# Performance work log

Hardware: AMD Instinct MI355X
Metric: run time of the kernel (lower is better)

## Reference

```python
import jax, jax.numpy as jnp
import numpy as np

B, C, H, W = 8, 2048, 14, 14
NUM_CLASSES, WORD_DIM, INTER_DIM = 80, 300, 1024


def setup_inputs() -> dict:
    key = jax.random.key(0)
    ks = jax.random.split(key, 8)
    s = 0.02
    return {
        "image_features": jax.random.normal(ks[0], (B, C, H, W), jnp.float32),
        "word_features": jax.random.normal(ks[1], (NUM_CLASSES, WORD_DIM), jnp.float32),
        "W1": jax.random.normal(ks[2], (INTER_DIM, C), jnp.float32) * s,
        "W2": jax.random.normal(ks[3], (INTER_DIM, WORD_DIM), jnp.float32) * s,
        "W3": jax.random.normal(ks[4], (INTER_DIM, INTER_DIM), jnp.float32) * s,
        "b3": jax.random.normal(ks[5], (INTER_DIM,), jnp.float32) * s,
        "Wa": jax.random.normal(ks[6], (1, INTER_DIM), jnp.float32) * s,
        "ba": jax.random.normal(ks[7], (1,), jnp.float32) * s,
        "num_classes": NUM_CLASSES,
    }


def reference(image_features, word_features, W1, W2, W3, b3, Wa, ba, num_classes):
    b, c, h, w = image_features.shape
    # [s, b, c] with s = h*w (spatial locations)
    img = image_features.reshape(b, c, h * w).transpose(2, 0, 1)
    f_wh = img @ W1.T                      # [s, b, D]
    f_wd = word_features @ W2.T            # [n, D]
    # additive-attention score MLP; broadcast to [s, b, n, D]
    lb = jnp.tanh(f_wh[:, :, None, :] * f_wd[None, None, :, :]) @ W3.T + b3
    coef = (lb @ Wa.T + ba)[..., 0]        # [s, b, n]
    coef = jax.nn.softmax(coef, axis=0)    # softmax over spatial locations
    # weighted sum over spatial dim -> [b, n, c]
    return jnp.einsum('sbc,sbn->bnc', img, coef)
```

## Files before the change

### kernel.cpp

```cpp
#include <hip/hip_runtime.h>
#include <math.h>

#define SB 196
#define SP 224
#define NB 8
#define NC 2048
#define ND 1024
#define NN 80
#define NW 300
#define CH 4
#define DCH (ND / CH)

typedef __bf16 v8bf __attribute__((ext_vector_type(8)));
typedef __bf16 v4bf __attribute__((ext_vector_type(4)));
typedef __bf16 v2bf __attribute__((ext_vector_type(2)));
typedef float  f32x4 __attribute__((ext_vector_type(4)));

__global__ __launch_bounds__(256) void k0_v(const float* __restrict__ W3,
                                            const float* __restrict__ Wa,
                                            float* __restrict__ v) {
    int d  = blockIdx.x * 256 + threadIdx.x;
    int e0 = blockIdx.y * 64;
    float p = 0.f;
    #pragma unroll 8
    for (int e = e0; e < e0 + 64; ++e) {
        p += Wa[e] * W3[(size_t)e * ND + d];
    }
    atomicAdd(&v[d], p);
}

__global__ __launch_bounds__(256) void k0_fwd(const float* __restrict__ word,
                                              const float* __restrict__ W2,
                                              const float* __restrict__ v,
                                              float2* __restrict__ wpack) {
    __shared__ __align__(16) float lword[NW];
    int n = blockIdx.x;
    int d = blockIdx.y * 256 + threadIdx.x;
    for (int i = threadIdx.x; i < NW; i += 256) lword[i] = word[(size_t)n * NW + i];
    __syncthreads();
    const float4* wr = (const float4*)(W2 + (size_t)d * NW);
    const float4* l4 = (const float4*)lword;
    float acc = 0.f;
    #pragma unroll 5
    for (int i = 0; i < NW / 4; ++i) {
        float4 a = wr[i], b = l4[i];
        acc += a.x * b.x + a.y * b.y + a.z * b.z + a.w * b.w;
    }
    float2 o;
    o.x = 2.8853900817779268f * acc;
    o.y = -2.f * v[d];
    wpack[(size_t)n * ND + d] = o;
}

__global__ __launch_bounds__(256) void kcast_w1(const float* __restrict__ W1,
                                                __bf16* __restrict__ O) {
    size_t i = ((size_t)blockIdx.x * 256 + threadIdx.x) * 4;
    float4 f = *(const float4*)(W1 + i);
    v4bf o;
    o[0] = (__bf16)f.x; o[1] = (__bf16)f.y; o[2] = (__bf16)f.z; o[3] = (__bf16)f.w;
    *(v4bf*)(O + i) = o;
}

__global__ __launch_bounds__(256) void kcast_x(const float* __restrict__ X,
                                               __bf16* __restrict__ Xt) {
    __shared__ float tile[64][65];
    const int b  = blockIdx.z;
    const int c0 = blockIdx.x * 64;
    const int s0 = blockIdx.y * 64;
    const int t  = threadIdx.x;
    const float* Xb = X + (size_t)b * NC * SB;
    {
        int ss = t & 63, cbase = t >> 6;
        #pragma unroll
        for (int r = 0; r < 16; ++r) {
            int cc = cbase + 4 * r;
            float val = (s0 + ss < SB) ? Xb[(size_t)(c0 + cc) * SB + s0 + ss] : 0.f;
            tile[cc][ss] = val;
        }
    }
    __syncthreads();
    {
        int cc = t & 63, sbase = t >> 6;
        #pragma unroll
        for (int r = 0; r < 16; ++r) {
            int ss = sbase + 4 * r;
            if (s0 + ss < SB)
                Xt[((size_t)b * SB + s0 + ss) * NC + c0 + cc] = (__bf16)tile[cc][ss];
        }
    }
}

#define PITCH 40
__global__ __launch_bounds__(256) void k1_mfma(const __bf16* __restrict__ Xt,
                                               const __bf16* __restrict__ W1b,
                                               float* __restrict__ F) {
    __shared__ __align__(16) __bf16 lA[64 * PITCH];
    __shared__ __align__(16) __bf16 lB[64 * PITCH];
    const int t    = threadIdx.x;
    const int d0   = blockIdx.x * 64;
    const int s0   = blockIdx.y * 64;
    const int b    = blockIdx.z;
    const int lane = t & 63;
    const int wave = t >> 6;
    const int doff = (wave & 1) * 32;
    const int soff = (wave >> 1) * 32;
    const int quad = lane >> 4;
    const int l16  = lane & 15;

    f32x4 acc[2][2] = {};

    const int rr = t >> 2;
    const int cc = (t & 3) * 8;
    const bool sv = (s0 + rr) < SB;
    const __bf16* Ag = W1b + (size_t)(d0 + rr) * NC + cc;
    const __bf16* Bg = Xt + ((size_t)b * SB + (sv ? (s0 + rr) : 0)) * NC + cc;
    __bf16* lAw = lA + rr * PITCH + cc;
    __bf16* lBw = lB + rr * PITCH + cc;

    const __bf16* rA0 = lA + (doff + l16) * PITCH + quad * 8;
    const __bf16* rA1 = rA0 + 16 * PITCH;
    const __bf16* rB0 = lB + (soff + l16) * PITCH + quad * 8;
    const __bf16* rB1 = rB0 + 16 * PITCH;

    for (int k0 = 0; k0 < NC; k0 += 32) {
        uint4 a = *(const uint4*)(Ag + k0);
        uint4 bv = sv ? *(const uint4*)(Bg + k0) : make_uint4(0u, 0u, 0u, 0u);
        __syncthreads();
        *(uint4*)lAw = a;
        *(uint4*)lBw = bv;
        __syncthreads();
        v8bf a0 = *(const v8bf*)rA0;
        v8bf a1 = *(const v8bf*)rA1;
        v8bf b0 = *(const v8bf*)rB0;
        v8bf b1 = *(const v8bf*)rB1;
        acc[0][0] = __builtin_amdgcn_mfma_f32_16x16x32_bf16(a0, b0, acc[0][0], 0, 0, 0);
        acc[0][1] = __builtin_amdgcn_mfma_f32_16x16x32_bf16(a0, b1, acc[0][1], 0, 0, 0);
        acc[1][0] = __builtin_amdgcn_mfma_f32_16x16x32_bf16(a1, b0, acc[1][0], 0, 0, 0);
        acc[1][1] = __builtin_amdgcn_mfma_f32_16x16x32_bf16(a1, b1, acc[1][1], 0, 0, 0);
    }
    float* Fb = F + (size_t)b * ND * SB;
    #pragma unroll
    for (int i = 0; i < 2; ++i) {
        #pragma unroll
        for (int j = 0; j < 2; ++j) {
            int s = s0 + soff + j * 16 + l16;
            if (s < SB) {
                #pragma unroll
                for (int r = 0; r < 4; ++r) {
                    int d = d0 + doff + i * 16 + quad * 4 + r;
                    Fb[(size_t)d * SB + s] = acc[i][j][r];
                }
            }
        }
    }
}

__global__ __launch_bounds__(256) void k2a(const float* __restrict__ F,
                                           const float2* __restrict__ wpack,
                                           float* __restrict__ part) {
    const int n  = blockIdx.x;
    const int b  = blockIdx.y;
    const int ch = blockIdx.z;
    const int t  = threadIdx.x;
    const int sc = (t < SB) ? t : (SB - 1);
    const float*  Fp = F + ((size_t)b * ND + ch * DCH) * SB + sc;
    const float2* wp = wpack + (size_t)n * ND + ch * DCH;
    float acc = 0.f;
    #pragma unroll 8
    for (int d = 0; d < DCH; ++d) {
        float2 w = wp[d];
        float x = Fp[(size_t)d * SB] * w.x;
        float e = __builtin_amdgcn_exp2f(x);
        float r = __builtin_amdgcn_rcpf(1.f + e);
        acc = fmaf(w.y, r, acc);
    }
    part[(((size_t)ch * NB + b) * NN + n) * 256 + t] = acc;
}

__global__ __launch_bounds__(256) void k2b(const float* __restrict__ part,
                                           __bf16* __restrict__ coefh,
                                           __bf16* __restrict__ coefl) {
    __shared__ float red[256];
    const int n = blockIdx.x;
    const int b = blockIdx.y;
    const int t = threadIdx.x;
    float acc = 0.f;
    #pragma unroll
    for (int ch = 0; ch < CH; ++ch)
        acc += part[(((size_t)ch * NB + b) * NN + n) * 256 + t];

    red[t] = (t < SB) ? acc : -1e30f;
    __syncthreads();
    #pragma unroll
    for (int off = 128; off > 0; off >>= 1) {
        if (t < off) red[t] = fmaxf(red[t], red[t + off]);
        __syncthreads();
    }
    float m = red[0];
    __syncthreads();
    float p = (t < SB) ? __expf(acc - m) : 0.f;
    red[t] = p;
    __syncthreads();
    #pragma unroll
    for (int off = 128; off > 0; off >>= 1) {
        if (t < off) red[t] += red[t + off];
        __syncthreads();
    }
    float inv = 1.f / red[0];
    if (t < SP) {
        float val = (t < SB) ? p * inv : 0.f;
        __bf16 h = (__bf16)val;
        __bf16 l = (__bf16)(val - (float)h);
        size_t base = ((size_t)b * NN + n) * SP + t;
        coefh[base] = h;
        coefl[base] = l;
    }
}

__global__ __launch_bounds__(256) void kcast_xs(const float* __restrict__ X,
                                                __bf16* __restrict__ Xhi,
                                                __bf16* __restrict__ Xlo) {
    unsigned int i = blockIdx.x * 256 + threadIdx.x;
    unsigned int row = i / 112;
    int s2 = (int)(i % 112) * 2;
    float x0 = 0.f, x1 = 0.f;
    if (s2 < SB) {
        float2 x = *(const float2*)(X + (size_t)row * SB + s2);
        x0 = x.x; x1 = x.y;
    }
    __bf16 h0 = (__bf16)x0, h1 = (__bf16)x1;
    __bf16 l0 = (__bf16)(x0 - (float)h0), l1 = (__bf16)(x1 - (float)h1);
    v2bf hv; hv[0] = h0; hv[1] = h1;
    v2bf lv; lv[0] = l0; lv[1] = l1;
    *(v2bf*)(Xhi + (size_t)row * SP + s2) = hv;
    *(v2bf*)(Xlo + (size_t)row * SP + s2) = lv;
}

__global__ __launch_bounds__(256) void k3_mfma(const __bf16* __restrict__ Xhi,
                                               const __bf16* __restrict__ Xlo,
                                               const __bf16* __restrict__ coefh,
                                               const __bf16* __restrict__ coefl,
                                               float* __restrict__ out) {
    const int t     = threadIdx.x;
    const int wave  = t >> 6;
    const int lane  = t & 63;
    const int quad  = lane >> 4;
    const int l16   = lane & 15;
    const int b     = blockIdx.y;
    const int cbase = blockIdx.x * 64 + wave * 16;

    const __bf16* Bh = Xhi + ((size_t)b * NC + cbase + l16) * SP + quad * 8;
    const __bf16* Bl = Xlo + ((size_t)b * NC + cbase + l16) * SP + quad * 8;
    const __bf16* Ah = coefh + ((size_t)b * NN + l16) * SP + quad * 8;
    const __bf16* Al = coefl + ((size_t)b * NN + l16) * SP + quad * 8;

    f32x4 acc[5] = {};

    #pragma unroll
    for (int k0 = 0; k0 < SP; k0 += 32) {
        v8bf bh = *(const v8bf*)(Bh + k0);
        v8bf bl = *(const v8bf*)(Bl + k0);
        #pragma unroll
        for (int mt = 0; mt < 5; ++mt) {
            v8bf ah = *(const v8bf*)(Ah + (size_t)mt * 16 * SP + k0);
            v8bf al = *(const v8bf*)(Al + (size_t)mt * 16 * SP + k0);
            acc[mt] = __builtin_amdgcn_mfma_f32_16x16x32_bf16(ah, bh, acc[mt], 0, 0, 0);
            acc[mt] = __builtin_amdgcn_mfma_f32_16x16x32_bf16(al, bh, acc[mt], 0, 0, 0);
            acc[mt] = __builtin_amdgcn_mfma_f32_16x16x32_bf16(ah, bl, acc[mt], 0, 0, 0);
        }
    }
    #pragma unroll
    for (int mt = 0; mt < 5; ++mt) {
        #pragma unroll
        for (int r = 0; r < 4; ++r) {
            int n = mt * 16 + quad * 4 + r;
            out[((size_t)b * NN + n) * NC + cbase + l16] = acc[mt][r];
        }
    }
}

extern "C" void kernel_launch(void* const* d_in, const int* in_sizes, int n_in,
                              void* d_out, int out_size, void* d_ws, size_t ws_size,
                              hipStream_t stream) {
    const float* X    = (const float*)d_in[0];
    const float* word = (const float*)d_in[1];
    const float* W1   = (const float*)d_in[2];
    const float* W2   = (const float*)d_in[3];
    const float* W3   = (const float*)d_in[4];
    const float* Wa   = (const float*)d_in[6];
    float* out = (float*)d_out;

    char* ws = (char*)d_ws;
    float*  v     = (float*)ws;
    float2* wpack = (float2*)(v + ND);
    float*  part  = (float*)(wpack + (size_t)NN * ND);
    __bf16* coefh = (__bf16*)(part + (size_t)CH * NB * NN * 256);
    __bf16* coefl = coefh + (size_t)NB * NN * SP;
    size_t big_off = ((size_t)((char*)(coefl + (size_t)NB * NN * SP) - ws) + 255) & ~(size_t)255;
    char* big = ws + big_off;
    __bf16* W1b = (__bf16*)big;
    __bf16* Xt  = W1b + (size_t)ND * NC;
    float*  F   = (float*)(Xt + (size_t)NB * SB * NC);
    __bf16* Xhi = (__bf16*)big;
    __bf16* Xlo = Xhi + (size_t)NB * NC * SP;

    hipMemsetAsync(v, 0, ND * sizeof(float), stream);
    k0_v    <<<dim3(4, 16),                 256, 0, stream>>>(W3, Wa, v);
    k0_fwd  <<<dim3(NN, 4),                 256, 0, stream>>>(word, W2, v, wpack);
    kcast_w1<<<dim3((ND * NC) / (256 * 4)), 256, 0, stream>>>(W1, W1b);
    kcast_x <<<dim3(32, 4, NB),             256, 0, stream>>>(X, Xt);
    k1_mfma <<<dim3(16, 4, NB),             256, 0, stream>>>(Xt, W1b, F);
    k2a     <<<dim3(NN, NB, CH),            256, 0, stream>>>(F, wpack, part);
    k2b     <<<dim3(NN, NB),                256, 0, stream>>>(part, coefh, coefl);
    kcast_xs<<<dim3((NB * NC * (SP / 2)) / 256), 256, 0, stream>>>(X, Xhi, Xlo);
    k3_mfma <<<dim3(NC / 64, NB),           256, 0, stream>>>(Xhi, Xlo, coefh, coefl, out);
}
```

Before: 198.9 us.

## Fuse hi/lo X split into transpose kernel and pack k2a threads densely

The bf16 hi/lo split of X is now produced inside the transposing cast kernel from the shared tile, which removes the separate kcast_xs pass and its extra read of X. k2a maps threads over flattened (batch, spatial) indices so no lanes sit idle on padding, and it loads weight pairs as float4 with a two-way unrolled inner loop. Xhi/Xlo no longer alias the W1b/Xt/F region, which increases workspace use.

```diff
diff --git a/kernel.cpp b/kernel.cpp
--- a/kernel.cpp
+++ b/kernel.cpp
@@ -62,7 +62,9 @@
 }
 
 __global__ __launch_bounds__(256) void kcast_x(const float* __restrict__ X,
-                                               __bf16* __restrict__ Xt) {
+                                               __bf16* __restrict__ Xt,
+                                               __bf16* __restrict__ Xhi,
+                                               __bf16* __restrict__ Xlo) {
     __shared__ float tile[64][65];
     const int b  = blockIdx.z;
     const int c0 = blockIdx.x * 64;
@@ -86,6 +88,22 @@
             int ss = sbase + 4 * r;
             if (s0 + ss < SB)
                 Xt[((size_t)b * SB + s0 + ss) * NC + c0 + cc] = (__bf16)tile[cc][ss];
+        }
+    }
+    {
+        int ss = t & 63, cbase = t >> 6;
+        int sg = s0 + ss;
+        #pragma unroll
+        for (int r = 0; r < 16; ++r) {
+            int cc = cbase + 4 * r;
+            if (sg < SP) {
+                float val = (sg < SB) ? tile[cc][ss] : 0.f;
+                __bf16 h = (__bf16)val;
+                __bf16 l = (__bf16)(val - (float)h);
+                size_t base = ((size_t)b * NC + c0 + cc) * SP + sg;
+                Xhi[base] = h;
+                Xlo[base] = l;
+            }
         }
     }
 }
@@ -158,23 +176,30 @@
 __global__ __launch_bounds__(256) void k2a(const float* __restrict__ F,
                                            const float2* __restrict__ wpack,
                                            float* __restrict__ part) {
-    const int n  = blockIdx.x;
-    const int b  = blockIdx.y;
-    const int ch = blockIdx.z;
-    const int t  = threadIdx.x;
-    const int sc = (t < SB) ? t : (SB - 1);
-    const float*  Fp = F + ((size_t)b * ND + ch * DCH) * SB + sc;
-    const float2* wp = wpack + (size_t)n * ND + ch * DCH;
+    const int n   = blockIdx.x;
+    const int ch  = blockIdx.z;
+    const int idx = blockIdx.y * 256 + threadIdx.x;
+    const bool valid = idx < (NB * SB);
+    const int iv = valid ? idx : 0;
+    const int b  = iv / SB;
+    const int s  = iv - b * SB;
+    const float*  Fp  = F + ((size_t)b * ND + ch * DCH) * SB + s;
+    const float4* wp4 = (const float4*)(wpack + (size_t)n * ND + ch * DCH);
     float acc = 0.f;
-    #pragma unroll 8
-    for (int d = 0; d < DCH; ++d) {
-        float2 w = wp[d];
-        float x = Fp[(size_t)d * SB] * w.x;
-        float e = __builtin_amdgcn_exp2f(x);
-        float r = __builtin_amdgcn_rcpf(1.f + e);
-        acc = fmaf(w.y, r, acc);
-    }
-    part[(((size_t)ch * NB + b) * NN + n) * 256 + t] = acc;
+    #pragma unroll 4
+    for (int d2 = 0; d2 < DCH / 2; ++d2) {
+        float4 w = wp4[d2];
+        float x0 = Fp[(size_t)(2 * d2)     * SB] * w.x;
+        float x1 = Fp[(size_t)(2 * d2 + 1) * SB] * w.z;
+        float e0 = __builtin_amdgcn_exp2f(x0);
+        float e1 = __builtin_amdgcn_exp2f(x1);
+        float r0 = __builtin_amdgcn_rcpf(1.f + e0);
+        float r1 = __builtin_amdgcn_rcpf(1.f + e1);
+        acc = fmaf(w.y, r0, acc);
+        acc = fmaf(w.w, r1, acc);
+    }
+    if (valid)
+        part[(((size_t)ch * NB + b) * NN + n) * 256 + s] = acc;
 }
 
 __global__ __launch_bounds__(256) void k2b(const float* __restrict__ part,
@@ -215,25 +240,6 @@
         coefh[base] = h;
         coefl[base] = l;
     }
-}
-
-__global__ __launch_bounds__(256) void kcast_xs(const float* __restrict__ X,
-                                                __bf16* __restrict__ Xhi,
-                                                __bf16* __restrict__ Xlo) {
-    unsigned int i = blockIdx.x * 256 + threadIdx.x;
-    unsigned int row = i / 112;
-    int s2 = (int)(i % 112) * 2;
-    float x0 = 0.f, x1 = 0.f;
-    if (s2 < SB) {
-        float2 x = *(const float2*)(X + (size_t)row * SB + s2);
-        x0 = x.x; x1 = x.y;
-    }
-    __bf16 h0 = (__bf16)x0, h1 = (__bf16)x1;
-    __bf16 l0 = (__bf16)(x0 - (float)h0), l1 = (__bf16)(x1 - (float)h1);
-    v2bf hv; hv[0] = h0; hv[1] = h1;
-    v2bf lv; lv[0] = l0; lv[1] = l1;
-    *(v2bf*)(Xhi + (size_t)row * SP + s2) = hv;
-    *(v2bf*)(Xlo + (size_t)row * SP + s2) = lv;
 }
 
 __global__ __launch_bounds__(256) void k3_mfma(const __bf16* __restrict__ Xhi,
@@ -296,22 +302,19 @@
     float*  part  = (float*)(wpack + (size_t)NN * ND);
     __bf16* coefh = (__bf16*)(part + (size_t)CH * NB * NN * 256);
     __bf16* coefl = coefh + (size_t)NB * NN * SP;
-    size_t big_off = ((size_t)((char*)(coefl + (size_t)NB * NN * SP) - ws) + 255) & ~(size_t)255;
-    char* big = ws + big_off;
-    __bf16* W1b = (__bf16*)big;
-    __bf16* Xt  = W1b + (size_t)ND * NC;
-    float*  F   = (float*)(Xt + (size_t)NB * SB * NC);
-    __bf16* Xhi = (__bf16*)big;
-    __bf16* Xlo = Xhi + (size_t)NB * NC * SP;
+    __bf16* W1b   = coefl + (size_t)NB * NN * SP;
+    __bf16* Xt    = W1b + (size_t)ND * NC;
+    float*  F     = (float*)(Xt + (size_t)NB * SB * NC);
+    __bf16* Xhi   = (__bf16*)(F + (size_t)NB * ND * SB);
+    __bf16* Xlo   = Xhi + (size_t)NB * NC * SP;
 
     hipMemsetAsync(v, 0, ND * sizeof(float), stream);
     k0_v    <<<dim3(4, 16),                 256, 0, stream>>>(W3, Wa, v);
     k0_fwd  <<<dim3(NN, 4),                 256, 0, stream>>>(word, W2, v, wpack);
     kcast_w1<<<dim3((ND * NC) / (256 * 4)), 256, 0, stream>>>(W1, W1b);
-    kcast_x <<<dim3(32, 4, NB),             256, 0, stream>>>(X, Xt);
+    kcast_x <<<dim3(32, 4, NB),             256, 0, stream>>>(X, Xt, Xhi, Xlo);
     k1_mfma <<<dim3(16, 4, NB),             256, 0, stream>>>(Xt, W1b, F);
-    k2a     <<<dim3(NN, NB, CH),            256, 0, stream>>>(F, wpack, part);
+    k2a     <<<dim3(NN, 7, CH),             256, 0, stream>>>(F, wpack, part);
     k2b     <<<dim3(NN, NB),                256, 0, stream>>>(part, coefh, coefl);
-    kcast_xs<<<dim3((NB * NC * (SP / 2)) / 256), 256, 0, stream>>>(X, Xhi, Xlo);
     k3_mfma <<<dim3(NC / 64, NB),           256, 0, stream>>>(Xhi, Xlo, coefh, coefl, out);
 }
```

Measured after the change: 192.5 us. 1.03x faster.
